# Kernel tuning notes

Hardware: AMD Instinct MI355X
Metric: run time of the kernel (lower is better)

Reference implementation:

```python
import jax, jax.numpy as jnp
import numpy as np

EMBED_DIM = 1024
NUM_HEADS = 8
PROJ_DIM = EMBED_DIM // NUM_HEADS  # 128
SIGMA = 1.0        # attn_param
DISP = 1           # attn_displacement
BATCH = 8
SEQ_LEN = 2048
# per-head hard-coded attention positions (length == num_heads)
POSITIONS = ['center', 'left', 'right', 'first', 'last', 'center', 'left', 'right']


def _head_centers(L):
    """Center of the analytic Gaussian per head and per query position. [H, L]"""
    i = jnp.arange(L, dtype=jnp.float32)
    centers = []
    for pos in POSITIONS:
        if pos == 'center':
            c = i
        elif pos == 'left':
            c = i - DISP
        elif pos == 'right':
            c = i + DISP
        elif pos == 'first':
            c = jnp.zeros_like(i)
        else:  # 'last' (no padding: last valid index is L-1)
            c = jnp.full_like(i, L - 1)
        centers.append(c)
    return jnp.stack(centers)  # [H, L]


def setup_inputs() -> dict:
    key = jax.random.key(0)
    k1, k2, k3 = jax.random.split(key, 3)
    x = jax.random.normal(k1, (BATCH, SEQ_LEN, EMBED_DIM), dtype=jnp.float32)
    # xavier-ish scale for square weights
    s = (6.0 / (EMBED_DIM + EMBED_DIM)) ** 0.5
    W_in = jax.random.uniform(k2, (EMBED_DIM, EMBED_DIM), dtype=jnp.float32, minval=-s, maxval=s)
    W_out = jax.random.uniform(k3, (EMBED_DIM, EMBED_DIM), dtype=jnp.float32, minval=-s, maxval=s)
    return {"x": x, "W_in": W_in, "W_out": W_out}


def reference(x, W_in, W_out):
    B, L, E = x.shape
    H, P = NUM_HEADS, PROJ_DIM
    # value projection (F.linear with input_weights), split into heads
    v = (x @ W_in.T).reshape(B, L, H, P).transpose(0, 2, 1, 3)  # [B, H, L, P]
    # analytic per-head attention weights: Gaussian in key-position around center
    j = jnp.arange(L, dtype=jnp.float32)
    c = _head_centers(L)                                         # [H, Lq]
    logits = -((j[None, None, :] - c[:, :, None]) ** 2) / (2.0 * SIGMA ** 2)  # [H, Lq, Lk]
    w = jax.nn.softmax(logits, axis=-1)                          # [H, Lq, Lk]
    # weighted value aggregation (torch.bmm(attn_weights, values) per head)
    attended = jnp.einsum('hqk,bhkp->bhqp', w, v)                # [B, H, L, P]
    attended = attended.transpose(0, 2, 1, 3).reshape(B, L, E)
    # bias-free output projection
    return attended @ W_out.T
```

## Files before the change

### kernel.cpp

```cpp
#include <hip/hip_runtime.h>
#include <stdint.h>

typedef unsigned short u16;
typedef unsigned int   u32;

typedef float  f32x4  __attribute__((ext_vector_type(4)));
typedef __bf16 bf16x8 __attribute__((ext_vector_type(8)));

__device__ __forceinline__ u16 f2bf(float f) {
  union { float f; u32 u; } c; c.f = f;
  u32 u = c.u + 0x7fffu + ((c.u >> 16) & 1u);
  return (u16)(u >> 16);
}
__device__ __forceinline__ float bf2f(u16 h) {
  union { u32 u; float f; } c; c.u = ((u32)h) << 16;
  return c.f;
}
__device__ __forceinline__ void gll16(const void* g, void* l) {
  __builtin_amdgcn_global_load_lds(
      (const __attribute__((address_space(1))) void*)g,
      (__attribute__((address_space(3))) void*)l, 16, 0, 0);
}

__global__ __launch_bounds__(256) void cvt_bf16(const float4* __restrict__ s,
                                                uint2* __restrict__ d, int n4) {
  int i = blockIdx.x * 256 + threadIdx.x;
  if (i >= n4) return;
  float4 v = s[i];
  uint2 o;
  o.x = (u32)f2bf(v.x) | ((u32)f2bf(v.y) << 16);
  o.y = (u32)f2bf(v.z) | ((u32)f2bf(v.w) << 16);
  d[i] = o;
}

__global__ __launch_bounds__(256) void cvt_bf16_w(const float4* __restrict__ s0,
                                                  uint2* __restrict__ d0,
                                                  const float4* __restrict__ s1,
                                                  uint2* __restrict__ d1, int n4) {
  int i = blockIdx.x * 256 + threadIdx.x;
  if (i >= n4) return;
  const float4* s = blockIdx.y ? s1 : s0;
  uint2*        d = blockIdx.y ? d1 : d0;
  float4 v = s[i];
  uint2 o;
  o.x = (u32)f2bf(v.x) | ((u32)f2bf(v.y) << 16);
  o.y = (u32)f2bf(v.z) | ((u32)f2bf(v.w) << 16);
  d[i] = o;
}

template <bool OUT_BF16>
__global__ __launch_bounds__(256, 4)
void gemm_nt_bf16(const u16* __restrict__ A, const u16* __restrict__ B,
                  void* __restrict__ Cout, int M, int N, int K) {
  __shared__ u16 As[128 * 32];
  __shared__ u16 Bs[128 * 32];
  const int t    = threadIdx.x;
  const int lane = t & 63;
  const int ml   = lane & 15;
  const int q    = lane >> 4;
  const int wave = t >> 6;
  const int wm   = wave >> 1;
  const int wn   = wave & 1;

  const int flat    = blockIdx.y * 8 + blockIdx.x;
  const int xcd     = flat & 7;
  const int slot    = flat >> 3;
  const int per_xcd = gridDim.y >> 3;
  const int mt      = xcd * per_xcd + (slot >> 3);
  const int nt      = slot & 7;
  const int m0      = mt * 128;
  const int n0      = nt * 128;

  f32x4 acc[4][4] = {};

  const int c1 = t + 256;
  const int r0 = t >> 2,  kk0 = (t & 3) * 8;
  const int r1 = c1 >> 2, kk1 = (c1 & 3) * 8;
  const u16* Ag0 = A + (size_t)(m0 + r0) * K + kk0;
  const u16* Ag1 = A + (size_t)(m0 + r1) * K + kk1;
  const u16* Bg0 = B + (size_t)(n0 + r0) * K + kk0;
  const u16* Bg1 = B + (size_t)(n0 + r1) * K + kk1;
  u16* AsW0 = As + (size_t)(t & 192) * 8;
  u16* AsW1 = As + (size_t)(256 + (t & 192)) * 8;
  u16* BsW0 = Bs + (size_t)(t & 192) * 8;
  u16* BsW1 = Bs + (size_t)(256 + (t & 192)) * 8;

  for (int k0 = 0; k0 < K; k0 += 32) {
    gll16(Ag0 + k0, AsW0);
    gll16(Ag1 + k0, AsW1);
    gll16(Bg0 + k0, BsW0);
    gll16(Bg1 + k0, BsW1);
    __syncthreads();
    bf16x8 af[4], bfv[4];
#pragma unroll
    for (int i = 0; i < 4; ++i)
      af[i] = *reinterpret_cast<const bf16x8*>(&As[(wm * 64 + i * 16 + ml) * 32 + q * 8]);
#pragma unroll
    for (int i = 0; i < 4; ++i)
      bfv[i] = *reinterpret_cast<const bf16x8*>(&Bs[(wn * 64 + i * 16 + ml) * 32 + q * 8]);
#pragma unroll
    for (int i = 0; i < 4; ++i)
#pragma unroll
      for (int j = 0; j < 4; ++j)
        acc[i][j] = __builtin_amdgcn_mfma_f32_16x16x32_bf16(af[i], bfv[j], acc[i][j], 0, 0, 0);
    __syncthreads();
  }

  const int rowb = m0 + wm * 64 + q * 4;
  const int colb = n0 + wn * 64 + ml;
#pragma unroll
  for (int i = 0; i < 4; ++i)
#pragma unroll
    for (int j = 0; j < 4; ++j)
#pragma unroll
      for (int r = 0; r < 4; ++r) {
        size_t idx = (size_t)(rowb + i * 16 + r) * N + (colb + j * 16);
        float val = acc[i][j][r];
        if (OUT_BF16) ((u16*)Cout)[idx] = f2bf(val);
        else          ((float*)Cout)[idx] = val;
      }
}

__global__ __launch_bounds__(256)
void gauss_conv(const u16* __restrict__ v, u16* __restrict__ att, int L) {
  constexpr float wt[13] = {
    1.5229979744712628e-08f, 3.7266531720786709e-06f, 3.3546262790251185e-04f,
    1.1108996538242306e-02f, 1.3533528323661270e-01f, 6.0653065971263342e-01f,
    1.0f,
    6.0653065971263342e-01f, 1.3533528323661270e-01f, 1.1108996538242306e-02f,
    3.3546262790251185e-04f, 3.7266531720786709e-06f, 1.5229979744712628e-08f
  };
  const int t  = threadIdx.x;
  const int fg = t & 15;
  const int li = t >> 4;
  const int l  = blockIdx.x * 16 + li;
  const int h  = blockIdx.y;
  const int b  = blockIdx.z;
  int c;
  switch (h) {
    case 0: case 5: c = l;     break;
    case 1: case 6: c = l - 1; break;
    case 2: case 7: c = l + 1; break;
    case 3:         c = 0;     break;
    default:        c = L - 1; break;
  }
  const int fbase = h * 128 + fg * 8;
  const u16* vb = v + (size_t)b * L * 1024 + fbase;

  float a[8] = {};
  float Z = 0.f;
#pragma unroll
  for (int d = -6; d <= 6; ++d) {
    int idx = c + d;
    bool ok = (idx >= 0) && (idx < L);
    int ic = idx < 0 ? 0 : (idx >= L ? L - 1 : idx);
    float w = ok ? wt[d + 6] : 0.f;
    Z += w;
    uint4 p = *reinterpret_cast<const uint4*>(vb + (size_t)ic * 1024);
    a[0] = fmaf(w, bf2f((u16)(p.x & 0xffffu)), a[0]);
    a[1] = fmaf(w, bf2f((u16)(p.x >> 16)),     a[1]);
    a[2] = fmaf(w, bf2f((u16)(p.y & 0xffffu)), a[2]);
    a[3] = fmaf(w, bf2f((u16)(p.y >> 16)),     a[3]);
    a[4] = fmaf(w, bf2f((u16)(p.z & 0xffffu)), a[4]);
    a[5] = fmaf(w, bf2f((u16)(p.z >> 16)),     a[5]);
    a[6] = fmaf(w, bf2f((u16)(p.w & 0xffffu)), a[6]);
    a[7] = fmaf(w, bf2f((u16)(p.w >> 16)),     a[7]);
  }
  float inv = 1.0f / Z;
  uint4 o;
  o.x = (u32)f2bf(a[0] * inv) | ((u32)f2bf(a[1] * inv) << 16);
  o.y = (u32)f2bf(a[2] * inv) | ((u32)f2bf(a[3] * inv) << 16);
  o.z = (u32)f2bf(a[4] * inv) | ((u32)f2bf(a[5] * inv) << 16);
  o.w = (u32)f2bf(a[6] * inv) | ((u32)f2bf(a[7] * inv) << 16);
  *reinterpret_cast<uint4*>(att + (size_t)(b * L + l) * 1024 + fbase) = o;
}

extern "C" void kernel_launch(void* const* d_in, const int* in_sizes, int n_in,
                              void* d_out, int out_size, void* d_ws, size_t ws_size,
                              hipStream_t stream) {
  const int Bb = 8, L = 2048, E = 1024;
  const int M = Bb * L, N = E, K = E;

  const float* x  = (const float*)d_in[0];
  const float* Wi = (const float*)d_in[1];
  const float* Wo = (const float*)d_in[2];
  float* out = (float*)d_out;

  size_t offV  = (size_t)M * E * 2;
  size_t offWi = offV + (size_t)M * E * 2;
  size_t offWo = offWi + (size_t)E * E * 2;
  size_t need  = offWo + (size_t)E * E * 2;
  if (ws_size < need) return;

  u16* xb  = (u16*)d_ws;
  u16* v   = (u16*)((char*)d_ws + offV);
  u16* wib = (u16*)((char*)d_ws + offWi);
  u16* wob = (u16*)((char*)d_ws + offWo);
  u16* att = xb;

  int n4x = M * E / 4, n4w = E * E / 4;
  cvt_bf16<<<n4x / 256, 256, 0, stream>>>((const float4*)x, (uint2*)xb, n4x);
  cvt_bf16_w<<<dim3(n4w / 256, 2), 256, 0, stream>>>(
      (const float4*)Wi, (uint2*)wib, (const float4*)Wo, (uint2*)wob, n4w);

  dim3 gg(N / 128, M / 128);
  gemm_nt_bf16<true ><<<gg, 256, 0, stream>>>(xb,  wib, v,   M, N, K);
  gauss_conv<<<dim3(L / 16, 8, Bb), 256, 0, stream>>>(v, att, L);
  gemm_nt_bf16<false><<<gg, 256, 0, stream>>>(att, wob, out, M, N, K);
}
```

Baseline: 221.9 us.

## Fuse fp32-to-bf16 conversion of x into first GEMM's LDS load path

Removes the standalone x conversion kernel. The first GEMM now loads fp32 x tiles straight into LDS and converts them to bf16 fragments in registers before the MFMA. The LDS layout of both GEMMs changes to a k-chunk-major arrangement, which changes the bank access pattern. The fused GEMM uses twice the LDS for A and issues twice the global loads per k-step, so occupancy and memory latency may suffer, but it avoids a full write and re-read of the bf16 copy of x.

```diff
diff --git a/kernel.cpp b/kernel.cpp
--- a/kernel.cpp
+++ b/kernel.cpp
@@ -21,16 +21,13 @@
       (const __attribute__((address_space(1))) void*)g,
       (__attribute__((address_space(3))) void*)l, 16, 0, 0);
 }
-
-__global__ __launch_bounds__(256) void cvt_bf16(const float4* __restrict__ s,
-                                                uint2* __restrict__ d, int n4) {
-  int i = blockIdx.x * 256 + threadIdx.x;
-  if (i >= n4) return;
-  float4 v = s[i];
-  uint2 o;
-  o.x = (u32)f2bf(v.x) | ((u32)f2bf(v.y) << 16);
-  o.y = (u32)f2bf(v.z) | ((u32)f2bf(v.w) << 16);
-  d[i] = o;
+__device__ __forceinline__ bf16x8 cvt8(f32x4 a, f32x4 b) {
+  union { u32 w[4]; bf16x8 v; } r;
+  r.w[0] = (u32)f2bf(a.x) | ((u32)f2bf(a.y) << 16);
+  r.w[1] = (u32)f2bf(a.z) | ((u32)f2bf(a.w) << 16);
+  r.w[2] = (u32)f2bf(b.x) | ((u32)f2bf(b.y) << 16);
+  r.w[3] = (u32)f2bf(b.z) | ((u32)f2bf(b.w) << 16);
+  return r.v;
 }
 
 __global__ __launch_bounds__(256) void cvt_bf16_w(const float4* __restrict__ s0,
@@ -48,10 +45,80 @@
   d[i] = o;
 }
 
-template <bool OUT_BF16>
 __global__ __launch_bounds__(256, 4)
-void gemm_nt_bf16(const u16* __restrict__ A, const u16* __restrict__ B,
-                  void* __restrict__ Cout, int M, int N, int K) {
+void gemm1_f32a(const float* __restrict__ A, const u16* __restrict__ B,
+                u16* __restrict__ C, int M, int N, int K) {
+  __shared__ float As[128 * 32];
+  __shared__ u16   Bs[128 * 32];
+  const int t    = threadIdx.x;
+  const int lane = t & 63;
+  const int ml   = lane & 15;
+  const int q    = lane >> 4;
+  const int wave = t >> 6;
+  const int wm   = wave >> 1;
+  const int wn   = wave & 1;
+
+  const int flat    = blockIdx.y * 8 + blockIdx.x;
+  const int xcd     = flat & 7;
+  const int slot    = flat >> 3;
+  const int per_xcd = gridDim.y >> 3;
+  const int mt      = xcd * per_xcd + (slot >> 3);
+  const int nt      = slot & 7;
+  const int m0      = mt * 128;
+  const int n0      = nt * 128;
+
+  f32x4 acc[4][4] = {};
+
+  const float* Aga = A + (size_t)(m0 + (t >> 1)) * K + 4 * (t & 1);
+  const u16*   Bga = B + (size_t)(n0 + (t >> 1)) * K + 8 * (t & 1);
+  const int wb = (t & 192) * 16;
+  char* AsB = (char*)As;
+  char* BsB = (char*)Bs;
+
+  for (int k0 = 0; k0 < K; k0 += 32) {
+#pragma unroll
+    for (int j = 0; j < 4; ++j)
+      gll16(Aga + k0 + 8 * j, AsB + j * 4096 + wb);
+#pragma unroll
+    for (int j = 0; j < 2; ++j)
+      gll16(Bga + k0 + 16 * j, BsB + j * 4096 + wb);
+    __syncthreads();
+
+    bf16x8 af[4], bfv[4];
+#pragma unroll
+    for (int i = 0; i < 4; ++i) {
+      const int R = wm * 64 + i * 16 + ml;
+      f32x4 a = *reinterpret_cast<const f32x4*>(&As[q * 1024 + R * 8]);
+      f32x4 b = *reinterpret_cast<const f32x4*>(&As[q * 1024 + R * 8 + 4]);
+      af[i] = cvt8(a, b);
+    }
+#pragma unroll
+    for (int i = 0; i < 4; ++i) {
+      const int R = wn * 64 + i * 16 + ml;
+      bfv[i] = *reinterpret_cast<const bf16x8*>(&Bs[(q >> 1) * 2048 + R * 16 + (q & 1) * 8]);
+    }
+#pragma unroll
+    for (int i = 0; i < 4; ++i)
+#pragma unroll
+      for (int j = 0; j < 4; ++j)
+        acc[i][j] = __builtin_amdgcn_mfma_f32_16x16x32_bf16(af[i], bfv[j], acc[i][j], 0, 0, 0);
+    __syncthreads();
+  }
+
+  const int rowb = m0 + wm * 64 + q * 4;
+  const int colb = n0 + wn * 64 + ml;
+#pragma unroll
+  for (int i = 0; i < 4; ++i)
+#pragma unroll
+    for (int j = 0; j < 4; ++j)
+#pragma unroll
+      for (int r = 0; r < 4; ++r)
+        C[(size_t)(rowb + i * 16 + r) * N + (colb + j * 16)] = f2bf(acc[i][j][r]);
+}
+
+__global__ __launch_bounds__(256, 4)
+void gemm2_bf16(const u16* __restrict__ A, const u16* __restrict__ B,
+                float* __restrict__ C, int M, int N, int K) {
   __shared__ u16 As[128 * 32];
   __shared__ u16 Bs[128 * 32];
   const int t    = threadIdx.x;
@@ -73,31 +140,31 @@
 
   f32x4 acc[4][4] = {};
 
-  const int c1 = t + 256;
-  const int r0 = t >> 2,  kk0 = (t & 3) * 8;
-  const int r1 = c1 >> 2, kk1 = (c1 & 3) * 8;
-  const u16* Ag0 = A + (size_t)(m0 + r0) * K + kk0;
-  const u16* Ag1 = A + (size_t)(m0 + r1) * K + kk1;
-  const u16* Bg0 = B + (size_t)(n0 + r0) * K + kk0;
-  const u16* Bg1 = B + (size_t)(n0 + r1) * K + kk1;
-  u16* AsW0 = As + (size_t)(t & 192) * 8;
-  u16* AsW1 = As + (size_t)(256 + (t & 192)) * 8;
-  u16* BsW0 = Bs + (size_t)(t & 192) * 8;
-  u16* BsW1 = Bs + (size_t)(256 + (t & 192)) * 8;
+  const u16* Aga = A + (size_t)(m0 + (t >> 1)) * K + 8 * (t & 1);
+  const u16* Bga = B + (size_t)(n0 + (t >> 1)) * K + 8 * (t & 1);
+  const int wb = (t & 192) * 16;
+  char* AsB = (char*)As;
+  char* BsB = (char*)Bs;
 
   for (int k0 = 0; k0 < K; k0 += 32) {
-    gll16(Ag0 + k0, AsW0);
-    gll16(Ag1 + k0, AsW1);
-    gll16(Bg0 + k0, BsW0);
-    gll16(Bg1 + k0, BsW1);
-    __syncthreads();
+#pragma unroll
+    for (int j = 0; j < 2; ++j) {
+      gll16(Aga + k0 + 16 * j, AsB + j * 4096 + wb);
+      gll16(Bga + k0 + 16 * j, BsB + j * 4096 + wb);
+    }
+    __syncthreads();
+
     bf16x8 af[4], bfv[4];
 #pragma unroll
-    for (int i = 0; i < 4; ++i)
-      af[i] = *reinterpret_cast<const bf16x8*>(&As[(wm * 64 + i * 16 + ml) * 32 + q * 8]);
-#pragma unroll
-    for (int i = 0; i < 4; ++i)
-      bfv[i] = *reinterpret_cast<const bf16x8*>(&Bs[(wn * 64 + i * 16 + ml) * 32 + q * 8]);
+    for (int i = 0; i < 4; ++i) {
+      const int R = wm * 64 + i * 16 + ml;
+      af[i] = *reinterpret_cast<const bf16x8*>(&As[(q >> 1) * 2048 + R * 16 + (q & 1) * 8]);
+    }
+#pragma unroll
+    for (int i = 0; i < 4; ++i) {
+      const int R = wn * 64 + i * 16 + ml;
+      bfv[i] = *reinterpret_cast<const bf16x8*>(&Bs[(q >> 1) * 2048 + R * 16 + (q & 1) * 8]);
+    }
 #pragma unroll
     for (int i = 0; i < 4; ++i)
 #pragma unroll
@@ -113,12 +180,8 @@
 #pragma unroll
     for (int j = 0; j < 4; ++j)
 #pragma unroll
-      for (int r = 0; r < 4; ++r) {
-        size_t idx = (size_t)(rowb + i * 16 + r) * N + (colb + j * 16);
-        float val = acc[i][j][r];
-        if (OUT_BF16) ((u16*)Cout)[idx] = f2bf(val);
-        else          ((float*)Cout)[idx] = val;
-      }
+      for (int r = 0; r < 4; ++r)
+        C[(size_t)(rowb + i * 16 + r) * N + (colb + j * 16)] = acc[i][j][r];
 }
 
 __global__ __launch_bounds__(256)
@@ -186,25 +249,23 @@
   const float* Wo = (const float*)d_in[2];
   float* out = (float*)d_out;
 
-  size_t offV  = (size_t)M * E * 2;
-  size_t offWi = offV + (size_t)M * E * 2;
-  size_t offWo = offWi + (size_t)E * E * 2;
-  size_t need  = offWo + (size_t)E * E * 2;
+  size_t offAtt = (size_t)M * E * 2;
+  size_t offWi  = offAtt + (size_t)M * E * 2;
+  size_t offWo  = offWi + (size_t)E * E * 2;
+  size_t need   = offWo + (size_t)E * E * 2;
   if (ws_size < need) return;
 
-  u16* xb  = (u16*)d_ws;
-  u16* v   = (u16*)((char*)d_ws + offV);
+  u16* v   = (u16*)d_ws;
+  u16* att = (u16*)((char*)d_ws + offAtt);
   u16* wib = (u16*)((char*)d_ws + offWi);
   u16* wob = (u16*)((char*)d_ws + offWo);
-  u16* att = xb;
-
-  int n4x = M * E / 4, n4w = E * E / 4;
-  cvt_bf16<<<n4x / 256, 256, 0, stream>>>((const float4*)x, (uint2*)xb, n4x);
+
+  int n4w = E * E / 4;
   cvt_bf16_w<<<dim3(n4w / 256, 2), 256, 0, stream>>>(
       (const float4*)Wi, (uint2*)wib, (const float4*)Wo, (uint2*)wob, n4w);
 
   dim3 gg(N / 128, M / 128);
-  gemm_nt_bf16<true ><<<gg, 256, 0, stream>>>(xb,  wib, v,   M, N, K);
+  gemm1_f32a<<<gg, 256, 0, stream>>>(x, wib, v, M, N, K);
   gauss_conv<<<dim3(L / 16, 8, Bb), 256, 0, stream>>>(v, att, L);
-  gemm_nt_bf16<false><<<gg, 256, 0, stream>>>(att, wob, out, M, N, K);
-}
+  gemm2_bf16<<<gg, 256, 0, stream>>>(att, wob, out, M, N, K);
+}
```

New measurement: 273.2 us. +23.1%, slower.

## Double GEMM K-tile to 64 with XOR-swizzled LDS and merge convert kernels

Applied to the files above, without the earlier changes.

The GEMM now loads a 64-wide K slice per iteration instead of 32, which halves the number of barrier pairs per tile and issues more MFMAs between syncs. The LDS layout uses an XOR swizzle on the 16-byte chunk index so fragment reads avoid bank conflicts. The three fp32-to-bf16 conversion launches are merged into one kernel. LDS use doubles to 32KB per block, which may limit occupancy at 4 blocks per CU.

```diff
diff --git a/kernel.cpp b/kernel.cpp
--- a/kernel.cpp
+++ b/kernel.cpp
@@ -22,38 +22,28 @@
       (__attribute__((address_space(3))) void*)l, 16, 0, 0);
 }
 
-__global__ __launch_bounds__(256) void cvt_bf16(const float4* __restrict__ s,
-                                                uint2* __restrict__ d, int n4) {
+__global__ __launch_bounds__(256)
+void cvt_all(const float4* __restrict__ x,  uint2* __restrict__ xb,  int n4x,
+             const float4* __restrict__ wi, uint2* __restrict__ wib,
+             const float4* __restrict__ wo, uint2* __restrict__ wob, int n4w) {
   int i = blockIdx.x * 256 + threadIdx.x;
-  if (i >= n4) return;
-  float4 v = s[i];
+  const float4* s; uint2* d; int j;
+  if (i < n4x)            { s = x;  d = xb;  j = i; }
+  else if (i < n4x + n4w) { s = wi; d = wib; j = i - n4x; }
+  else                    { s = wo; d = wob; j = i - n4x - n4w; }
+  float4 v = s[j];
   uint2 o;
   o.x = (u32)f2bf(v.x) | ((u32)f2bf(v.y) << 16);
   o.y = (u32)f2bf(v.z) | ((u32)f2bf(v.w) << 16);
-  d[i] = o;
-}
-
-__global__ __launch_bounds__(256) void cvt_bf16_w(const float4* __restrict__ s0,
-                                                  uint2* __restrict__ d0,
-                                                  const float4* __restrict__ s1,
-                                                  uint2* __restrict__ d1, int n4) {
-  int i = blockIdx.x * 256 + threadIdx.x;
-  if (i >= n4) return;
-  const float4* s = blockIdx.y ? s1 : s0;
-  uint2*        d = blockIdx.y ? d1 : d0;
-  float4 v = s[i];
-  uint2 o;
-  o.x = (u32)f2bf(v.x) | ((u32)f2bf(v.y) << 16);
-  o.y = (u32)f2bf(v.z) | ((u32)f2bf(v.w) << 16);
-  d[i] = o;
+  d[j] = o;
 }
 
 template <bool OUT_BF16>
 __global__ __launch_bounds__(256, 4)
 void gemm_nt_bf16(const u16* __restrict__ A, const u16* __restrict__ B,
                   void* __restrict__ Cout, int M, int N, int K) {
-  __shared__ u16 As[128 * 32];
-  __shared__ u16 Bs[128 * 32];
+  __shared__ u16 As[128 * 64];
+  __shared__ u16 Bs[128 * 64];
   const int t    = threadIdx.x;
   const int lane = t & 63;
   const int ml   = lane & 15;
@@ -73,36 +63,42 @@
 
   f32x4 acc[4][4] = {};
 
-  const int c1 = t + 256;
-  const int r0 = t >> 2,  kk0 = (t & 3) * 8;
-  const int r1 = c1 >> 2, kk1 = (c1 & 3) * 8;
-  const u16* Ag0 = A + (size_t)(m0 + r0) * K + kk0;
-  const u16* Ag1 = A + (size_t)(m0 + r1) * K + kk1;
-  const u16* Bg0 = B + (size_t)(n0 + r0) * K + kk0;
-  const u16* Bg1 = B + (size_t)(n0 + r1) * K + kk1;
-  u16* AsW0 = As + (size_t)(t & 192) * 8;
-  u16* AsW1 = As + (size_t)(256 + (t & 192)) * 8;
-  u16* BsW0 = Bs + (size_t)(t & 192) * 8;
-  u16* BsW1 = Bs + (size_t)(256 + (t & 192)) * 8;
-
-  for (int k0 = 0; k0 < K; k0 += 32) {
-    gll16(Ag0 + k0, AsW0);
-    gll16(Ag1 + k0, AsW1);
-    gll16(Bg0 + k0, BsW0);
-    gll16(Bg1 + k0, BsW1);
+  const int sr = t >> 3;
+  const int gk = (((t & 7) ^ (sr & 7)) * 8);
+  const u16* Ag = A + (size_t)(m0 + sr) * K + gk;
+  const u16* Bg = B + (size_t)(n0 + sr) * K + gk;
+  const int wb = (t & 192) * 16;
+  char* AsB = (char*)As;
+  char* BsB = (char*)Bs;
+
+  for (int k0 = 0; k0 < K; k0 += 64) {
+#pragma unroll
+    for (int j = 0; j < 4; ++j) {
+      gll16(Ag + (size_t)(32 * j) * K + k0, AsB + j * 4096 + wb);
+      gll16(Bg + (size_t)(32 * j) * K + k0, BsB + j * 4096 + wb);
+    }
     __syncthreads();
-    bf16x8 af[4], bfv[4];
-#pragma unroll
-    for (int i = 0; i < 4; ++i)
-      af[i] = *reinterpret_cast<const bf16x8*>(&As[(wm * 64 + i * 16 + ml) * 32 + q * 8]);
-#pragma unroll
-    for (int i = 0; i < 4; ++i)
-      bfv[i] = *reinterpret_cast<const bf16x8*>(&Bs[(wn * 64 + i * 16 + ml) * 32 + q * 8]);
-#pragma unroll
-    for (int i = 0; i < 4; ++i)
-#pragma unroll
-      for (int j = 0; j < 4; ++j)
-        acc[i][j] = __builtin_amdgcn_mfma_f32_16x16x32_bf16(af[i], bfv[j], acc[i][j], 0, 0, 0);
+#pragma unroll
+    for (int s = 0; s < 2; ++s) {
+      bf16x8 af[4], bfv[4];
+#pragma unroll
+      for (int i = 0; i < 4; ++i) {
+        const int R = wm * 64 + i * 16 + ml;
+        af[i] = *reinterpret_cast<const bf16x8*>(
+            &As[R * 64 + (((s * 4 + q) ^ (R & 7)) * 8)]);
+      }
+#pragma unroll
+      for (int i = 0; i < 4; ++i) {
+        const int R = wn * 64 + i * 16 + ml;
+        bfv[i] = *reinterpret_cast<const bf16x8*>(
+            &Bs[R * 64 + (((s * 4 + q) ^ (R & 7)) * 8)]);
+      }
+#pragma unroll
+      for (int i = 0; i < 4; ++i)
+#pragma unroll
+        for (int j = 0; j < 4; ++j)
+          acc[i][j] = __builtin_amdgcn_mfma_f32_16x16x32_bf16(af[i], bfv[j], acc[i][j], 0, 0, 0);
+    }
     __syncthreads();
   }
 
@@ -199,9 +195,10 @@
   u16* att = xb;
 
   int n4x = M * E / 4, n4w = E * E / 4;
-  cvt_bf16<<<n4x / 256, 256, 0, stream>>>((const float4*)x, (uint2*)xb, n4x);
-  cvt_bf16_w<<<dim3(n4w / 256, 2), 256, 0, stream>>>(
-      (const float4*)Wi, (uint2*)wib, (const float4*)Wo, (uint2*)wob, n4w);
+  int nblk = (n4x + 2 * n4w) / 256;
+  cvt_all<<<nblk, 256, 0, stream>>>((const float4*)x, (uint2*)xb, n4x,
+                                    (const float4*)Wi, (uint2*)wib,
+                                    (const float4*)Wo, (uint2*)wob, n4w);
 
   dim3 gg(N / 128, M / 128);
   gemm_nt_bf16<true ><<<gg, 256, 0, stream>>>(xb,  wib, v,   M, N, K);
```

Result: faster. 210.6 us (-5.1%).
